# Kernel tuning notes

Measured on AMD Instinct MI355X. Metric: run time of the kernel, lower is better.

The kernel has to match this reference:

```python
import jax, jax.numpy as jnp
import numpy as np
from jax import lax

G = 1000  # hard-coded grid size in ConvCNP.forward
LOG_2PI = float(np.log(2.0 * np.pi))


def _conv1d(x, w, b):
    # x: (B, Cin, L), w: (Cout, Cin, K), SAME padding, stride 1 (k=5, pad=2)
    y = lax.conv_general_dilated(x, w, (1,), 'SAME',
                                 dimension_numbers=('NCH', 'OIH', 'NCH'))
    return y + b[None, :, None]


def setup_inputs() -> dict:
    key = jax.random.key(0)
    ks = jax.random.split(key, 16)
    B, Nc, Nt = 32, 2048, 2048
    inp = {
        'x_context': jax.random.normal(ks[0], (B, 1, Nc), jnp.float32),
        'y_context': jax.random.normal(ks[1], (B, 1, Nc), jnp.float32),
        'x_target': jax.random.normal(ks[2], (B, 1, Nt), jnp.float32),
        'y_target': jax.random.normal(ks[3], (B, 1, Nt), jnp.float32),
        # learned kernel lengthscales (nn.Parameter init 0.5)
        'ls_x': jnp.asarray(0.5, jnp.float32),
        'ls_rho': jnp.asarray(0.5, jnp.float32),
        # SimpleCNN(2, 1): channels [2, 16, 32, 16, 2], k=5
        'W1': 0.1 * jax.random.normal(ks[4], (16, 2, 5), jnp.float32),
        'b1': jnp.zeros((16,), jnp.float32),
        'W2': 0.1 * jax.random.normal(ks[5], (32, 16, 5), jnp.float32),
        'b2': jnp.zeros((32,), jnp.float32),
        'W3': 0.1 * jax.random.normal(ks[6], (16, 32, 5), jnp.float32),
        'b3': jnp.zeros((16,), jnp.float32),
        'W4': 0.1 * jax.random.normal(ks[7], (2, 16, 5), jnp.float32),
        'b4': jnp.zeros((2,), jnp.float32),
    }
    return inp


def _forward(x_context, y_context, x_target, y_target,
             ls_x, ls_rho, W1, b1, W2, b2, W3, b3, W4, b4):
    B = x_context.shape[0]
    xc = x_context[:, 0, :]            # (B, Nc)
    xt = x_target[:, 0, :]             # (B, Nt)
    t = jnp.linspace(-2.2, 2.2, G).astype(x_context.dtype)  # (G,)

    # phi(y) = [1, y] density/signal channels: (B, 2, Nc)
    phi = jnp.concatenate([jnp.ones_like(y_context), y_context], axis=1)

    # EQ-kernel interpolation context -> grid: w[b,g,n] = exp(-(t_g-x_n)^2/(2 l^2))
    d2 = (t[None, :, None] - xc[:, None, :]) ** 2           # (B, G, Nc)
    w_x = jnp.exp(-d2 / (2.0 * ls_x * ls_x))
    h = jnp.einsum('bgn,bcn->bcg', w_x, phi)                # (B, 2, G)

    density = h[:, 0:1, :]
    rest = h[:, 1:, :] / (density + 1e-8)
    h = jnp.concatenate([density, rest], axis=1)            # (B, 2, G)

    # SimpleCNN
    y = jax.nn.relu(_conv1d(h, W1, b1))
    y = jax.nn.relu(_conv1d(y, W2, b2))
    y = jax.nn.relu(_conv1d(y, W3, b3))
    y = _conv1d(y, W4, b4)                                  # (B, 2, G)
    y_mu_grid = y[:, 0:1, :]
    y_sigma_grid = jax.nn.softplus(y[:, 1:2, :])
    y_grid = jnp.concatenate([y_mu_grid, y_sigma_grid], axis=1)  # (B, 2, G)

    # EQ-kernel interpolation grid -> targets
    d2t = (xt[:, :, None] - t[None, None, :]) ** 2          # (B, Nt, G)
    w_rho = jnp.exp(-d2t / (2.0 * ls_rho * ls_rho))
    y_pred = jnp.einsum('btg,bcg->bct', w_rho, y_grid)      # (B, 2, Nt)

    mu = y_pred[:, 0:1, :]
    sigma = y_pred[:, 1:2, :]

    # Normal(mu, sigma).log_prob(y_target), mean over points, sum over batch
    z = (y_target - mu) / sigma
    logp = -0.5 * z * z - jnp.log(sigma) - 0.5 * LOG_2PI    # (B, 1, Nt)
    loss = -jnp.sum(jnp.mean(logp, axis=-1))
    return mu.transpose(0, 2, 1), sigma.transpose(0, 2, 1), loss


def reference(x_context, y_context, x_target, y_target,
              ls_x, ls_rho, W1, b1, W2, b2, W3, b3, W4, b4):
    return _forward(x_context, y_context, x_target, y_target,
                    ls_x, ls_rho, W1, b1, W2, b2, W3, b3, W4, b4)
```

## Files before the change

kernel.cpp:

```cpp
#include <hip/hip_runtime.h>
#include <math.h>

#define G     1000
#define B     32
#define NC    2048
#define NT    2048
#define BN    (B * NT)
#define LOG2E 1.4426950408889634f
#define LN2PI 1.8378770664093453f

#if __has_builtin(__builtin_amdgcn_exp2f)
#define EXP2F(x) __builtin_amdgcn_exp2f(x)
#else
#define EXP2F(x) exp2f(x)
#endif

__global__ __launch_bounds__(512) void k_smooth(
    const float* __restrict__ xc, const float* __restrict__ yc,
    const float* __restrict__ ls_x, float* __restrict__ h,
    float* __restrict__ loss_slot) {
  __shared__ float sxy[NC * 2];
  __shared__ float pA0[512], pA1[512], pB0[512], pB1[512];
  if (blockIdx.x == 0 && blockIdx.y == 0 && threadIdx.x == 0) *loss_slot = 0.f;

  int tid = threadIdx.x;
  int b = blockIdx.y, tile = blockIdx.x;
  float ls = ls_x[0];
  float s  = sqrtf(0.5f * LOG2E) / ls;

  const float* xb = xc + b * NC;
  const float* yb = yc + b * NC;
  for (int n = tid; n < NC; n += 512) {
    sxy[2 * n]     = s * xb[n];
    sxy[2 * n + 1] = yb[n];
  }
  __syncthreads();

  int lane = tid & 63, wv = tid >> 6;
  int ga = tile * 128 + lane;
  float step = s * (4.4f / 999.f);
  float tga = s * -2.2f + step * (float)ga;
  float tgb = tga + step * 64.f;

  float a0 = 0.f, a1 = 0.f, b0 = 0.f, b1 = 0.f;
  const float4* p = ((const float4*)sxy) + wv * (NC / 16);
  #pragma unroll 4
  for (int i = 0; i < NC / 16; ++i) {
    float4 v = p[i];
    float d, w;
    d = tga - v.x; w = EXP2F(-(d * d)); a0 += w; a1 = fmaf(w, v.y, a1);
    d = tgb - v.x; w = EXP2F(-(d * d)); b0 += w; b1 = fmaf(w, v.y, b1);
    d = tga - v.z; w = EXP2F(-(d * d)); a0 += w; a1 = fmaf(w, v.w, a1);
    d = tgb - v.z; w = EXP2F(-(d * d)); b0 += w; b1 = fmaf(w, v.w, b1);
  }
  pA0[tid] = a0; pA1[tid] = a1; pB0[tid] = b0; pB1[tid] = b1;
  __syncthreads();

  if (tid < 128) {
    int which = tid >> 6, l = tid & 63;
    int g = tile * 128 + which * 64 + l;
    if (g < G) {
      const float* q0 = which ? pB0 : pA0;
      const float* q1 = which ? pB1 : pA1;
      float d0 = 0.f, d1 = 0.f;
      #pragma unroll
      for (int k = 0; k < 8; ++k) { d0 += q0[l + 64 * k]; d1 += q1[l + 64 * k]; }
      h[(b * 2 + 0) * G + g] = d0;
      h[(b * 2 + 1) * G + g] = d1 / (d0 + 1e-8f);
    }
  }
}

#define TILE  48
#define NTILE 21
#define CSTR  68

template <int CIN, int COUT, int WSTR, int NPASS>
__device__ __forceinline__ void conv_layer5(
    const float* __restrict__ in, float* __restrict__ out,
    const float* __restrict__ wt, const float* __restrict__ bias, int tid) {
  #pragma unroll
  for (int pass = 0; pass < NPASS; ++pass) {
    int idx = tid + pass * 256;
    int oc  = idx % COUT;
    int i0  = (idx / COUT) * 4;
    float acc[4];
    float bb = bias[oc];
    #pragma unroll
    for (int p = 0; p < 4; ++p) acc[p] = bb;
    for (int ic = 0; ic < CIN; ++ic) {
      const float* ip = in + ic * CSTR + i0;
      float4 va = *(const float4*)ip;
      float4 vb = *(const float4*)(ip + 4);
      float v[8] = {va.x, va.y, va.z, va.w, vb.x, vb.y, vb.z, vb.w};
      const float* wp = wt + oc * WSTR + ic * 5;
      float w[5];
      #pragma unroll
      for (int k = 0; k < 5; ++k) w[k] = wp[k];
      #pragma unroll
      for (int p = 0; p < 4; ++p)
        #pragma unroll
        for (int k = 0; k < 5; ++k)
          acc[p] = fmaf(v[p + k], w[k], acc[p]);
    }
    float* op = out + oc * CSTR + i0 + 2;
    *(float2*)op       = make_float2(fmaxf(acc[0], 0.f), fmaxf(acc[1], 0.f));
    *(float2*)(op + 2) = make_float2(fmaxf(acc[2], 0.f), fmaxf(acc[3], 0.f));
  }
}

__global__ __launch_bounds__(256, 4) void k_conv(
    const float* __restrict__ h,
    const float* __restrict__ W1, const float* __restrict__ Bs1,
    const float* __restrict__ W2, const float* __restrict__ Bs2,
    const float* __restrict__ W3, const float* __restrict__ Bs3,
    const float* __restrict__ W4, const float* __restrict__ Bs4,
    float* __restrict__ yg) {
  __shared__ __align__(16) float bufA[32 * CSTR], bufB[32 * CSTR];
  __shared__ float wt1[176], wt2[2592], wt3[2576], wt4[162];
  __shared__ float sB1[16], sB2[32], sB3[16], sB4[2];

  int tid  = threadIdx.x;
  int tile = blockIdx.x, b = blockIdx.y;
  int ts   = tile * TILE;

  for (int i = tid; i < 160;  i += 256) wt1[(i / 10)  * 11  + i % 10]  = W1[i];
  for (int i = tid; i < 2560; i += 256) wt2[(i / 80)  * 81  + i % 80]  = W2[i];
  for (int i = tid; i < 2560; i += 256) wt3[(i / 160) * 161 + i % 160] = W3[i];
  for (int i = tid; i < 160;  i += 256) wt4[(i / 80)  * 81  + i % 80]  = W4[i];
  if (tid < 16)       sB1[tid]      = Bs1[tid];
  else if (tid < 48)  sB2[tid - 16] = Bs2[tid - 16];
  else if (tid < 64)  sB3[tid - 48] = Bs3[tid - 48];
  else if (tid < 66)  sB4[tid - 64] = Bs4[tid - 64];

  for (int i = tid; i < 2 * CSTR; i += 256) {
    int c = i >= CSTR, col = i - c * CSTR;
    int g = ts + col - 10;
    bufA[c * CSTR + col] = (g >= 0 && g < G) ? h[(b * 2 + c) * G + g] : 0.f;
  }
  __syncthreads();

  conv_layer5<2, 16, 11, 1>(bufA, bufB, wt1, sB1, tid);
  __syncthreads();
  conv_layer5<16, 32, 81, 2>(bufB, bufA, wt2, sB2, tid);
  __syncthreads();
  conv_layer5<32, 16, 161, 1>(bufA, bufB, wt3, sB3, tid);
  __syncthreads();

  if (tid < 96) {
    int oc = tid >= 48;
    int j  = tid - oc * 48;
    int i  = 10 + j;
    float sacc = sB4[oc];
    #pragma unroll
    for (int ic = 0; ic < 16; ++ic) {
      const float* ip = bufB + ic * CSTR + i - 2;
      #pragma unroll
      for (int k = 0; k < 5; ++k)
        sacc = fmaf(ip[k], wt4[oc * 81 + ic * 5 + k], sacc);
    }
    int gp = ts + j;
    if (gp < G) {
      if (oc == 0) {
        yg[(b * 2 + 0) * G + gp] = sacc;
      } else {
        float sp_ = fmaxf(sacc, 0.f) + log1pf(__expf(-fabsf(sacc)));
        yg[(b * 2 + 1) * G + gp] = sp_;
      }
    }
  }
}

__global__ __launch_bounds__(512) void k_pred(
    const float* __restrict__ xt, const float* __restrict__ yt,
    const float* __restrict__ ls_rho, const float* __restrict__ yg,
    float* __restrict__ out) {
  __shared__ float2 sp[G];
  __shared__ float pA0[512], pA1[512], pB0[512], pB1[512];
  __shared__ float red[8];

  int tid = threadIdx.x;
  int b = blockIdx.y, tile = blockIdx.x;
  float ls = ls_rho[0];
  float s  = sqrtf(0.5f * LOG2E) / ls;
  float dl = s * (4.4f / 999.f);

  const float* y0 = yg + (b * 2 + 0) * G;
  const float* y1 = yg + (b * 2 + 1) * G;
  for (int g = tid; g < G; g += 512) sp[g] = make_float2(y0[g], y1[g]);
  __syncthreads();

  int lane = tid & 63, wv = tid >> 6;
  int ta = tile * 128 + lane;
  float ua = s * xt[b * NT + ta];
  float ub = s * xt[b * NT + ta + 64];
  float base = 2.2f * s - dl * (float)(wv * 125);
  float aa = ua + base, ab = ub + base;
  float Wa = EXP2F(64.f - aa * aa), qa = EXP2F(dl * (aa + aa) - dl * dl);
  float Wb = EXP2F(64.f - ab * ab), qb = EXP2F(dl * (ab + ab) - dl * dl);
  float r  = EXP2F(-2.f * dl * dl);

  float muA = 0.f, sgA = 0.f, muB = 0.f, sgB = 0.f;
  const float2* p = sp + wv * 125;
  #pragma unroll 5
  for (int i = 0; i < 125; ++i) {
    float2 v = p[i];
    muA = fmaf(Wa, v.x, muA); sgA = fmaf(Wa, v.y, sgA); Wa *= qa; qa *= r;
    muB = fmaf(Wb, v.x, muB); sgB = fmaf(Wb, v.y, sgB); Wb *= qb; qb *= r;
  }
  pA0[tid] = muA; pA1[tid] = sgA; pB0[tid] = muB; pB1[tid] = sgB;
  __syncthreads();

  float lp = 0.f;
  if (tid < 128) {
    int which = tid >> 6, l = tid & 63;
    int t = tile * 128 + which * 64 + l;
    const float* q0 = which ? pB0 : pA0;
    const float* q1 = which ? pB1 : pA1;
    float mu = 0.f, sg = 0.f;
    #pragma unroll
    for (int k = 0; k < 8; ++k) { mu += q0[l + 64 * k]; sg += q1[l + 64 * k]; }
    mu *= 0x1p-64f;
    sg *= 0x1p-64f;
    out[b * NT + t]      = mu;
    out[BN + b * NT + t] = sg;
    float z = (yt[b * NT + t] - mu) / sg;
    lp = -0.5f * z * z - __logf(sg) - 0.5f * LN2PI;
  }
  #pragma unroll
  for (int m = 32; m; m >>= 1) lp += __shfl_xor(lp, m);
  if ((tid & 63) == 0) red[tid >> 6] = lp;
  __syncthreads();
  if (tid == 0) {
    float tot = 0.f;
    #pragma unroll
    for (int i = 0; i < 8; ++i) tot += red[i];
    atomicAdd(out + 2 * BN, -tot * (1.f / (float)NT));
  }
}

extern "C" void kernel_launch(void* const* d_in, const int* in_sizes, int n_in,
                              void* d_out, int out_size, void* d_ws, size_t ws_size,
                              hipStream_t stream) {
  const float* xc  = (const float*)d_in[0];
  const float* yc  = (const float*)d_in[1];
  const float* xt  = (const float*)d_in[2];
  const float* yt  = (const float*)d_in[3];
  const float* lsx = (const float*)d_in[4];
  const float* lsr = (const float*)d_in[5];
  const float* W1  = (const float*)d_in[6];  const float* b1 = (const float*)d_in[7];
  const float* W2  = (const float*)d_in[8];  const float* b2 = (const float*)d_in[9];
  const float* W3  = (const float*)d_in[10]; const float* b3 = (const float*)d_in[11];
  const float* W4  = (const float*)d_in[12]; const float* b4 = (const float*)d_in[13];

  float* out = (float*)d_out;
  float* h   = (float*)d_ws;
  float* yg  = h + B * 2 * G;

  k_smooth<<<dim3(8, B), 512, 0, stream>>>(xc, yc, lsx, h, out + 2 * BN);
  k_conv<<<dim3(NTILE, B), 256, 0, stream>>>(h, W1, b1, W2, b2, W3, b3, W4, b4, yg);
  k_pred<<<dim3(16, B), 512, 0, stream>>>(xt, yt, lsr, yg, out);
}
```

Baseline: 44.52 us.

## Widen conv register tiles to 8 outputs and pack grid pairs into float4

The conv layers now compute 8 outputs per thread instead of 4, with weights repacked into a float4 plus a transposed scalar for the fifth tap. This is meant to cut LDS reads per FMA, and occupancy is lowered to 2 blocks per CU to allow more registers. The prediction kernel pads the grid to 1024 points stored as float4 pairs, so each wave reads 128 points in 64 wide LDS loads. The padded zeros contribute nothing to the sums, but waves now process uneven real work.

Result: no change. 43.92 us (-1.4%).

```diff
diff --git a/kernel.cpp b/kernel.cpp
--- a/kernel.cpp
+++ b/kernel.cpp
@@ -75,41 +75,37 @@
 #define NTILE 21
 #define CSTR  68
 
-template <int CIN, int COUT, int WSTR, int NPASS>
-__device__ __forceinline__ void conv_layer5(
+template <int CIN, int COUT, int S4>
+__device__ __forceinline__ void conv8(
     const float* __restrict__ in, float* __restrict__ out,
-    const float* __restrict__ wt, const float* __restrict__ bias, int tid) {
-  #pragma unroll
-  for (int pass = 0; pass < NPASS; ++pass) {
-    int idx = tid + pass * 256;
-    int oc  = idx % COUT;
-    int i0  = (idx / COUT) * 4;
-    float acc[4];
+    const float4* __restrict__ wf4, const float* __restrict__ w4p,
+    const float* __restrict__ bias, int tid) {
+  if (tid < COUT * 8) {
+    int oc = tid % COUT;
+    int i0 = (tid / COUT) * 8;
+    float acc[8];
     float bb = bias[oc];
     #pragma unroll
-    for (int p = 0; p < 4; ++p) acc[p] = bb;
+    for (int p = 0; p < 8; ++p) acc[p] = bb;
     for (int ic = 0; ic < CIN; ++ic) {
-      const float* ip = in + ic * CSTR + i0;
-      float4 va = *(const float4*)ip;
-      float4 vb = *(const float4*)(ip + 4);
-      float v[8] = {va.x, va.y, va.z, va.w, vb.x, vb.y, vb.z, vb.w};
-      const float* wp = wt + oc * WSTR + ic * 5;
-      float w[5];
+      const float4* ip = (const float4*)(in + ic * CSTR + i0);
+      float4 A = ip[0], Bv = ip[1], C = ip[2];
+      float v[12] = {A.x, A.y, A.z, A.w, Bv.x, Bv.y, Bv.z, Bv.w, C.x, C.y, C.z, C.w};
+      float4 w = wf4[oc * S4 + ic];
+      float w4v = w4p[ic * COUT + oc];
       #pragma unroll
-      for (int k = 0; k < 5; ++k) w[k] = wp[k];
-      #pragma unroll
-      for (int p = 0; p < 4; ++p)
-        #pragma unroll
-        for (int k = 0; k < 5; ++k)
-          acc[p] = fmaf(v[p + k], w[k], acc[p]);
+      for (int p = 0; p < 8; ++p)
+        acc[p] = fmaf(v[p], w.x, fmaf(v[p+1], w.y, fmaf(v[p+2], w.z,
+                 fmaf(v[p+3], w.w, fmaf(v[p+4], w4v, acc[p])))));
     }
     float* op = out + oc * CSTR + i0 + 2;
-    *(float2*)op       = make_float2(fmaxf(acc[0], 0.f), fmaxf(acc[1], 0.f));
-    *(float2*)(op + 2) = make_float2(fmaxf(acc[2], 0.f), fmaxf(acc[3], 0.f));
-  }
-}
-
-__global__ __launch_bounds__(256, 4) void k_conv(
+    #pragma unroll
+    for (int j = 0; j < 4; ++j)
+      *(float2*)(op + 2 * j) = make_float2(fmaxf(acc[2*j], 0.f), fmaxf(acc[2*j+1], 0.f));
+  }
+}
+
+__global__ __launch_bounds__(256, 2) void k_conv(
     const float* __restrict__ h,
     const float* __restrict__ W1, const float* __restrict__ Bs1,
     const float* __restrict__ W2, const float* __restrict__ Bs2,
@@ -117,17 +113,31 @@
     const float* __restrict__ W4, const float* __restrict__ Bs4,
     float* __restrict__ yg) {
   __shared__ __align__(16) float bufA[32 * CSTR], bufB[32 * CSTR];
-  __shared__ float wt1[176], wt2[2592], wt3[2576], wt4[162];
-  __shared__ float sB1[16], sB2[32], sB3[16], sB4[2];
+  __shared__ float4 wf1[16 * 3], wf2[32 * 17], wf3[16 * 33];
+  __shared__ float  w41[2 * 16], w42[16 * 32], w43[32 * 16];
+  __shared__ float  wt4[162];
+  __shared__ float  sB1[16], sB2[32], sB3[16], sB4[2];
 
   int tid  = threadIdx.x;
   int tile = blockIdx.x, b = blockIdx.y;
   int ts   = tile * TILE;
 
-  for (int i = tid; i < 160;  i += 256) wt1[(i / 10)  * 11  + i % 10]  = W1[i];
-  for (int i = tid; i < 2560; i += 256) wt2[(i / 80)  * 81  + i % 80]  = W2[i];
-  for (int i = tid; i < 2560; i += 256) wt3[(i / 160) * 161 + i % 160] = W3[i];
-  for (int i = tid; i < 160;  i += 256) wt4[(i / 80)  * 81  + i % 80]  = W4[i];
+  if (tid < 32) {
+    int oc = tid >> 1, ic = tid & 1, a = oc * 10 + ic * 5;
+    wf1[oc * 3 + ic] = make_float4(W1[a], W1[a+1], W1[a+2], W1[a+3]);
+    w41[ic * 16 + oc] = W1[a + 4];
+  }
+  for (int pr = tid; pr < 512; pr += 256) {
+    int oc = pr >> 4, ic = pr & 15, a = oc * 80 + ic * 5;
+    wf2[oc * 17 + ic] = make_float4(W2[a], W2[a+1], W2[a+2], W2[a+3]);
+    w42[ic * 32 + oc] = W2[a + 4];
+  }
+  for (int pr = tid; pr < 512; pr += 256) {
+    int oc = pr >> 5, ic = pr & 31, a = oc * 160 + ic * 5;
+    wf3[oc * 33 + ic] = make_float4(W3[a], W3[a+1], W3[a+2], W3[a+3]);
+    w43[ic * 16 + oc] = W3[a + 4];
+  }
+  for (int i = tid; i < 160; i += 256) wt4[(i / 80) * 81 + i % 80] = W4[i];
   if (tid < 16)       sB1[tid]      = Bs1[tid];
   else if (tid < 48)  sB2[tid - 16] = Bs2[tid - 16];
   else if (tid < 64)  sB3[tid - 48] = Bs3[tid - 48];
@@ -140,11 +150,11 @@
   }
   __syncthreads();
 
-  conv_layer5<2, 16, 11, 1>(bufA, bufB, wt1, sB1, tid);
-  __syncthreads();
-  conv_layer5<16, 32, 81, 2>(bufB, bufA, wt2, sB2, tid);
-  __syncthreads();
-  conv_layer5<32, 16, 161, 1>(bufA, bufB, wt3, sB3, tid);
+  conv8<2, 16, 3>(bufA, bufB, wf1, w41, sB1, tid);
+  __syncthreads();
+  conv8<16, 32, 17>(bufB, bufA, wf2, w42, sB2, tid);
+  __syncthreads();
+  conv8<32, 16, 33>(bufA, bufB, wf3, w43, sB3, tid);
   __syncthreads();
 
   if (tid < 96) {
@@ -175,7 +185,7 @@
     const float* __restrict__ xt, const float* __restrict__ yt,
     const float* __restrict__ ls_rho, const float* __restrict__ yg,
     float* __restrict__ out) {
-  __shared__ float2 sp[G];
+  __shared__ float4 sp[512];
   __shared__ float pA0[512], pA1[512], pB0[512], pB1[512];
   __shared__ float red[8];
 
@@ -187,26 +197,33 @@
 
   const float* y0 = yg + (b * 2 + 0) * G;
   const float* y1 = yg + (b * 2 + 1) * G;
-  for (int g = tid; g < G; g += 512) sp[g] = make_float2(y0[g], y1[g]);
+  {
+    int g0 = 2 * tid, g1 = 2 * tid + 1;
+    float a0 = (g0 < G) ? y0[g0] : 0.f, b0_ = (g0 < G) ? y1[g0] : 0.f;
+    float a1 = (g1 < G) ? y0[g1] : 0.f, b1_ = (g1 < G) ? y1[g1] : 0.f;
+    sp[tid] = make_float4(a0, b0_, a1, b1_);
+  }
   __syncthreads();
 
   int lane = tid & 63, wv = tid >> 6;
   int ta = tile * 128 + lane;
   float ua = s * xt[b * NT + ta];
   float ub = s * xt[b * NT + ta + 64];
-  float base = 2.2f * s - dl * (float)(wv * 125);
+  float base = 2.2f * s - dl * (float)(wv * 128);
   float aa = ua + base, ab = ub + base;
   float Wa = EXP2F(64.f - aa * aa), qa = EXP2F(dl * (aa + aa) - dl * dl);
   float Wb = EXP2F(64.f - ab * ab), qb = EXP2F(dl * (ab + ab) - dl * dl);
   float r  = EXP2F(-2.f * dl * dl);
 
   float muA = 0.f, sgA = 0.f, muB = 0.f, sgB = 0.f;
-  const float2* p = sp + wv * 125;
-  #pragma unroll 5
-  for (int i = 0; i < 125; ++i) {
-    float2 v = p[i];
+  const float4* p = sp + wv * 64;
+  #pragma unroll 4
+  for (int i = 0; i < 64; ++i) {
+    float4 v = p[i];
     muA = fmaf(Wa, v.x, muA); sgA = fmaf(Wa, v.y, sgA); Wa *= qa; qa *= r;
     muB = fmaf(Wb, v.x, muB); sgB = fmaf(Wb, v.y, sgB); Wb *= qb; qb *= r;
+    muA = fmaf(Wa, v.z, muA); sgA = fmaf(Wa, v.w, sgA); Wa *= qa; qa *= r;
+    muB = fmaf(Wb, v.z, muB); sgB = fmaf(Wb, v.w, sgB); Wb *= qb; qb *= r;
   }
   pA0[tid] = muA; pA1[tid] = sgA; pB0[tid] = muB; pB1[tid] = sgB;
   __syncthreads();
```
